# Performance work log

Measured on AMD Instinct MI355X. Metric: run time of the kernel, lower is better.

## Reference

```python
import jax, jax.numpy as jnp
import numpy as np

BANDWIDTH = 512.0


def _pairwise_lse(A, B, bandwidth):
    """logsumexp over all pairs of exp(-||a-b||^2 / bandwidth).

    Matches torch: vmap over rows b of B computing logsumexp over A,
    then logsumexp over those row results == single logsumexp over the
    full [Na, Nb] matrix of -sq_dist/bandwidth.
    """
    # squared distances via ||a||^2 + ||b||^2 - 2 a.b  (GEMM-dominated)
    a2 = jnp.sum(A * A, axis=-1)  # [Na]
    b2 = jnp.sum(B * B, axis=-1)  # [Nb]
    d2 = a2[:, None] + b2[None, :] - 2.0 * (A @ B.T)  # [Na, Nb]
    return jax.nn.logsumexp(-d2 / bandwidth)


def setup_inputs() -> dict:
    key = jax.random.key(0)
    kx, ky = jax.random.split(key)
    X = jax.random.normal(kx, (8192, 512), dtype=jnp.float32)
    Y = jax.random.normal(ky, (8192, 512), dtype=jnp.float32)
    return {"X": X, "Y": Y}


def reference(X, Y):
    n = X.shape[0]
    m = Y.shape[0]
    xx = (jnp.exp(_pairwise_lse(X, X, BANDWIDTH)) - n) / (n * (n - 1))
    xy = jnp.exp(_pairwise_lse(X, Y, BANDWIDTH)) / (n * m)
    yy = (jnp.exp(_pairwise_lse(Y, Y, BANDWIDTH)) - m) / (m * (m - 1))
    return xx - 2.0 * xy + yy
```

## Files before the change

### kernel.cpp

```cpp
#include <hip/hip_runtime.h>
#include <math.h>


#define D      512
#define BTM    128
#define BTN    256
#define BK     16
#define KSTEPS (D / BK)

#define AHI 0
#define ALO 256
#define BHI 512
#define BLO 1024

typedef _Float16 half8 __attribute__((ext_vector_type(8)));
typedef __attribute__((ext_vector_type(8)))  short  short8;
typedef __attribute__((ext_vector_type(16))) float  f32x16;

union U4H8 { uint4 u; half8 h; };
union U4S8 { uint4 u; short8 s; };

__device__ __forceinline__ unsigned short bf16_rne(float x) {
    unsigned u = __float_as_uint(x);
    return (unsigned short)((u + 0x7fffu + ((u >> 16) & 1u)) >> 16);
}
__device__ __forceinline__ float bf16_f32(unsigned short b) {
    return __uint_as_float(((unsigned)b) << 16);
}
__device__ __forceinline__ void split8(const float v[8], uint4& hi, uint4& lo) {
    unsigned h[8], l[8];
    #pragma unroll
    for (int j = 0; j < 8; j++) {
        unsigned short bh = bf16_rne(v[j]);
        float r = v[j] - bf16_f32(bh);
        unsigned short bl = bf16_rne(r);
        h[j] = bh; l[j] = bl;
    }
    hi.x = h[0] | (h[1] << 16); hi.y = h[2] | (h[3] << 16);
    hi.z = h[4] | (h[5] << 16); hi.w = h[6] | (h[7] << 16);
    lo.x = l[0] | (l[1] << 16); lo.y = l[2] | (l[3] << 16);
    lo.z = l[4] | (l[5] << 16); lo.w = l[6] | (l[7] << 16);
}

__device__ __forceinline__ void lds16(const uint4* g, uint4* l) {
    __builtin_amdgcn_global_load_lds(
        (const __attribute__((address_space(1))) void*)g,
        (__attribute__((address_space(3))) void*)(unsigned int)(uintptr_t)(void*)l,
        16, 0, 0);
}

__global__ __launch_bounds__(256)
void convert_h_kernel(const float* __restrict__ src, uint4* __restrict__ dst, int npts) {
    const int ks = blockIdx.y;
    const int p  = blockIdx.x * 256 + threadIdx.x;
    if (p >= npts) return;
    const float* s = src + (size_t)p * D + ks * BK;
    float v[16];
    *(float4*)&v[0]  = *(const float4*)(s);
    *(float4*)&v[4]  = *(const float4*)(s + 4);
    *(float4*)&v[8]  = *(const float4*)(s + 8);
    *(float4*)&v[12] = *(const float4*)(s + 12);
    U4H8 a, b;
    #pragma unroll
    for (int j = 0; j < 8; j++) { a.h[j] = (_Float16)v[j]; b.h[j] = (_Float16)v[8 + j]; }
    size_t u = (size_t)ks * npts * 2 + (size_t)(p >> 5) * 64 + (p & 31);
    dst[u] = a.u; dst[u + 32] = b.u;
}

__global__ __launch_bounds__(256)
void row_norms_kernel(const float* __restrict__ X, const float* __restrict__ Y,
                      float* __restrict__ X2, float* __restrict__ Y2, int N, int M) {
    const int wave = threadIdx.x >> 6;
    const int lane = threadIdx.x & 63;
    const int row  = blockIdx.x * 4 + wave;
    const float* src; float* dst; int r;
    if (row < N)          { src = X; dst = X2; r = row; }
    else if (row < N + M) { src = Y; dst = Y2; r = row - N; }
    else return;
    const float* p = src + (size_t)r * D;
    float s = 0.f;
    #pragma unroll
    for (int c = 0; c < D; c += 64) {
        float v = p[c + lane];
        s = fmaf(v, v, s);
    }
    #pragma unroll
    for (int off = 32; off > 0; off >>= 1) s += __shfl_down(s, off);
    if (lane == 0) dst[r] = s;
}

__device__ inline unsigned float_key(float f) {
    unsigned u = __float_as_uint(f);
    return (u & 0x80000000u) ? ~u : (u | 0x80000000u);
}
__device__ inline float key_float(unsigned k) {
    return __uint_as_float((k & 0x80000000u) ? (k ^ 0x80000000u) : ~k);
}

__global__ __launch_bounds__(256)
void diag_min_bits_kernel(const float* __restrict__ src, const float* __restrict__ n2,
                          unsigned* __restrict__ minkey, int zidx) {
    const int tid  = threadIdx.x;
    const int wave = tid >> 6, lane = tid & 63;
    const int grp  = blockIdx.x * 4 + wave;
    const int fp   = lane & 31, fh = lane >> 5;
    const int pt   = grp * 32 + fp;
    const float* s = src + (size_t)pt * D + fh * 8;

    f32x16 acc;
    #pragma unroll
    for (int i = 0; i < 16; i++) acc[i] = 0.f;

    for (int ks = 0; ks < KSTEPS; ks++) {
        float v[8];
        *(float4*)&v[0] = *(const float4*)(s + ks * BK);
        *(float4*)&v[4] = *(const float4*)(s + ks * BK + 4);
        U4S8 hi, lo;
        split8(v, hi.u, lo.u);
        short8 ah = hi.s, al = lo.s;
        acc = __builtin_amdgcn_mfma_f32_32x32x16_bf16(ah, ah, acc, 0, 0, 0);
        acc = __builtin_amdgcn_mfma_f32_32x32x16_bf16(ah, al, acc, 0, 0, 0);
        acc = __builtin_amdgcn_mfma_f32_32x32x16_bf16(al, ah, acc, 0, 0, 0);
    }

    float dmin = 1e30f;
    if (fh == ((fp >> 2) & 1)) {
        int r = (fp & 3) + 4 * (fp >> 3);
        float av = acc[r];
        float rn = n2[pt];
        float cn = rn;
        float d2 = rn + cn - 2.0f * av;
        dmin = d2;
    }
    #pragma unroll
    for (int off = 32; off > 0; off >>= 1) dmin = fminf(dmin, __shfl_down(dmin, off));
    __shared__ float wm[4];
    if (lane == 0) wm[wave] = dmin;
    __syncthreads();
    if (tid == 0)
        atomicMin(&minkey[zidx],
                  float_key(fminf(fminf(wm[0], wm[1]), fminf(wm[2], wm[3]))));
}

struct AF { half8 h[2]; };

__global__ __launch_bounds__(256, 2)
void pair_exp_sum_kernel(const uint4* __restrict__ Xh, const uint4* __restrict__ Yh,
                         const float* __restrict__ X2, const float* __restrict__ Y2,
                         double* __restrict__ accum, float* __restrict__ bmin,
                         int N, int M) {
    const int z = blockIdx.z;
    const uint4 *Ah, *Bh; const float *An, *Bn; bool sym; int na, nb;
    if (z == 0)      { Ah = Xh; Bh = Xh; An = X2; Bn = X2; sym = true;  na = N; nb = N; }
    else if (z == 1) { Ah = Xh; Bh = Yh; An = X2; Bn = Y2; sym = false; na = N; nb = M; }
    else             { Ah = Yh; Bh = Yh; An = Y2; Bn = Y2; sym = true;  na = M; nb = M; }
    const int bi = blockIdx.x, bj = blockIdx.y;
    if (sym && (2 * bj + 1) < bi) return;

    __shared__ uint4  smem[2][512];
    __shared__ float  smN[BTM + BTN];
    __shared__ double wsum[4];
    __shared__ float  wmin[4];

    const int tid  = threadIdx.x;
    const int wave = tid >> 6, lane = tid & 63;
    const int wy = wave >> 1, wx = wave & 1;
    const int row0 = bi * BTM, col0 = bj * BTN;

    if (tid < BTM) smN[tid] = An[row0 + tid];
    smN[BTM + tid] = Bn[col0 + tid];

    const int wl = wave * 64 + lane;
    const size_t strideA = (size_t)na * 2;
    const size_t strideB = (size_t)nb * 2;
    const uint4* gB0 = Bh + (size_t)(col0 >> 5) * 64 + wl;
    const uint4* gB1 = gB0 + 256;
    const half8* gA0 = (const half8*)Ah + ((size_t)(row0 >> 5) + 2 * wy) * 64 + lane;
    const half8* gA1 = gA0 + 64;

    f32x16 acc[2][4];
    #pragma unroll
    for (int g = 0; g < 2; g++)
        #pragma unroll
        for (int c = 0; c < 4; c++)
            #pragma unroll
            for (int i = 0; i < 16; i++) acc[g][c][i] = 0.f;

    auto stage = [&](int buf, int ks) {
        lds16(gB0 + (size_t)ks * strideB, &smem[buf][wl]);
        lds16(gB1 + (size_t)ks * strideB, &smem[buf][256 + wl]);
    };
    auto loadA = [&](int ks, AF& f) {
        f.h[0] = gA0[(size_t)ks * strideA];
        f.h[1] = gA1[(size_t)ks * strideA];
    };
    auto compute = [&](int buf, const AF& a) {
        const half8* p = (const half8*)&smem[buf][0];
        half8 bh[4];
        #pragma unroll
        for (int c = 0; c < 4; c++) bh[c] = p[(4 * wx + c) * 64 + lane];
        #pragma unroll
        for (int g = 0; g < 2; g++)
            #pragma unroll
            for (int c = 0; c < 4; c++)
                acc[g][c] = __builtin_amdgcn_mfma_f32_32x32x16_f16(a.h[g], bh[c], acc[g][c], 0, 0, 0);
    };

    AF A0, A1;
    stage(0, 0);
    loadA(0, A0);
    __syncthreads();

    for (int ks = 1; ks < KSTEPS - 1; ks += 2) {
        stage(1, ks);      loadA(ks, A1);
        compute(0, A0);
        __syncthreads();
        stage(0, ks + 1);  loadA(ks + 1, A0);
        compute(1, A1);
        __syncthreads();
    }
    stage(1, KSTEPS - 1);  loadA(KSTEPS - 1, A1);
    compute(0, A0);
    __syncthreads();
    compute(1, A1);

    float wgt = 1.f;
    if (sym) {
        int cblk = 2 * bj + wx;
        wgt = (cblk > bi) ? 2.f : (cblk == bi ? 1.f : 0.f);
    }

    const int fp = lane & 31, fh = lane >> 5;
    double s = 0.0;
    float dmin = 1e30f;
    if (wgt != 0.f) {
        const float* rowN = &smN[64 * wy];
        const float* colN = &smN[BTM + 128 * wx];
        const float kC = -0.0028177637517362567f;
        #pragma unroll
        for (int g = 0; g < 2; g++)
            #pragma unroll
            for (int c = 0; c < 4; c++) {
                float cn = colN[32 * c + fp];
                float rs = 0.f;
                #pragma unroll
                for (int r = 0; r < 16; r++) {
                    int r32 = (r & 3) + 8 * (r >> 2) + 4 * fh;
                    float d2 = rowN[32 * g + r32] + cn - 2.0f * acc[g][c][r];
                    dmin = fminf(dmin, d2);
                    rs += exp2f(d2 * kC);
                }
                s += (double)rs;
            }
        s *= (double)wgt;
    }

    #pragma unroll
    for (int off = 32; off > 0; off >>= 1) {
        s += __shfl_down(s, off);
        dmin = fminf(dmin, __shfl_down(dmin, off));
    }
    if (lane == 0) { wsum[wave] = s; wmin[wave] = dmin; }
    __syncthreads();
    if (tid == 0) {
        atomicAdd(&accum[z], wsum[0] + wsum[1] + wsum[2] + wsum[3]);
        if (z == 1)
            bmin[bi * gridDim.y + bj] = fminf(fminf(wmin[0], wmin[1]),
                                              fminf(wmin[2], wmin[3]));
    }
}

__global__ __launch_bounds__(256)
void xy_gmin_kernel(const float* __restrict__ bmin, float* __restrict__ gmin, int nblk) {
    float m = 1e30f;
    for (int i = threadIdx.x; i < nblk; i += 256) m = fminf(m, bmin[i]);
    #pragma unroll
    for (int off = 32; off > 0; off >>= 1) m = fminf(m, __shfl_down(m, off));
    __shared__ float wm[4];
    if ((threadIdx.x & 63) == 0) wm[threadIdx.x >> 6] = m;
    __syncthreads();
    if (threadIdx.x == 0) gmin[0] = fminf(fminf(wm[0], wm[1]), fminf(wm[2], wm[3]));
}

__global__ __launch_bounds__(256)
void refine_min_kernel(const float* __restrict__ A, const float* __restrict__ B,
                       const float* __restrict__ An, const float* __restrict__ Bn,
                       const float* __restrict__ bmin, const float* __restrict__ gmin,
                       unsigned* __restrict__ minkey, int zidx) {
    const int bi = blockIdx.x;
    const int bj = blockIdx.y;
    if (!(bmin[bi * gridDim.y + bj] < gmin[0] + 0.5f)) return;
    const int row0 = bi * BTM, col0 = bj * BTN;

    __shared__ uint4 smem[1536];
    __shared__ float smN[BTM + BTN];
    __shared__ float wmin[4];

    const int tid  = threadIdx.x;
    const int wave = tid >> 6, lane = tid & 63;
    const int wy = wave >> 1, wx = wave & 1;
    if (tid < BTM) smN[tid] = An[row0 + tid];
    smN[BTM + tid] = Bn[col0 + tid];

    const int fp = lane & 31, fh = lane >> 5;
    int au[2], bu[4];
    #pragma unroll
    for (int g = 0; g < 2; g++) au[g] = (64 * wy + 32 * g + fp) * 2 + fh;
    #pragma unroll
    for (int c = 0; c < 4; c++) bu[c] = (128 * wx + 32 * c + fp) * 2 + fh;

    f32x16 acc[2][4];
    #pragma unroll
    for (int g = 0; g < 2; g++)
        #pragma unroll
        for (int c = 0; c < 4; c++)
            #pragma unroll
            for (int i = 0; i < 16; i++) acc[g][c][i] = 0.f;

    for (int ks = 0; ks < KSTEPS; ks++) {
        __syncthreads();
        {
            const float* s = A + (size_t)(row0 + (tid >> 1)) * D + ks * BK + (tid & 1) * 8;
            float v[8];
            *(float4*)&v[0] = *(const float4*)s;
            *(float4*)&v[4] = *(const float4*)(s + 4);
            uint4 hi, lo; split8(v, hi, lo);
            smem[AHI + tid] = hi; smem[ALO + tid] = lo;
        }
        #pragma unroll
        for (int t = 0; t < 2; t++) {
            int u = tid + t * 256;
            const float* s = B + (size_t)(col0 + (u >> 1)) * D + ks * BK + (u & 1) * 8;
            float v[8];
            *(float4*)&v[0] = *(const float4*)s;
            *(float4*)&v[4] = *(const float4*)(s + 4);
            uint4 hi, lo; split8(v, hi, lo);
            smem[BHI + u] = hi; smem[BLO + u] = lo;
        }
        __syncthreads();
        {
            const short8* p = (const short8*)&smem[0];
            short8 ah[2], al[2], bh[4], bl[4];
            #pragma unroll
            for (int g = 0; g < 2; g++) { ah[g] = p[AHI + au[g]]; al[g] = p[ALO + au[g]]; }
            #pragma unroll
            for (int c = 0; c < 4; c++) { bh[c] = p[BHI + bu[c]]; bl[c] = p[BLO + bu[c]]; }
            #pragma unroll
            for (int g = 0; g < 2; g++)
                #pragma unroll
                for (int c = 0; c < 4; c++)
                    acc[g][c] = __builtin_amdgcn_mfma_f32_32x32x16_bf16(ah[g], bh[c], acc[g][c], 0, 0, 0);
            #pragma unroll
            for (int g = 0; g < 2; g++)
                #pragma unroll
                for (int c = 0; c < 4; c++)
                    acc[g][c] = __builtin_amdgcn_mfma_f32_32x32x16_bf16(ah[g], bl[c], acc[g][c], 0, 0, 0);
            #pragma unroll
            for (int g = 0; g < 2; g++)
                #pragma unroll
                for (int c = 0; c < 4; c++)
                    acc[g][c] = __builtin_amdgcn_mfma_f32_32x32x16_bf16(al[g], bh[c], acc[g][c], 0, 0, 0);
        }
    }

    float dmin = 1e30f;
    const float* rowN = &smN[64 * wy];
    const float* colN = &smN[BTM + 128 * wx];
    #pragma unroll
    for (int g = 0; g < 2; g++)
        #pragma unroll
        for (int c = 0; c < 4; c++) {
            float cn = colN[32 * c + fp];
            #pragma unroll
            for (int r = 0; r < 16; r++) {
                int r32 = (r & 3) + 8 * (r >> 2) + 4 * fh;
                float d2 = rowN[32 * g + r32] + cn - 2.0f * acc[g][c][r];
                dmin = fminf(dmin, d2);
            }
        }

    #pragma unroll
    for (int off = 32; off > 0; off >>= 1) dmin = fminf(dmin, __shfl_down(dmin, off));
    if (lane == 0) wmin[wave] = dmin;
    __syncthreads();
    if (tid == 0)
        atomicMin(&minkey[zidx],
                  float_key(fminf(fminf(wmin[0], wmin[1]), fminf(wmin[2], wmin[3]))));
}

__global__ void finalize_kernel(const double* __restrict__ accum,
                                const unsigned* __restrict__ minkey,
                                float* __restrict__ out, int N, int M) {
    if (threadIdx.x == 0 && blockIdx.x == 0) {
        float Sp[3];
        #pragma unroll
        for (int z = 0; z < 3; z++) {
            float m = key_float(minkey[z]) * (-1.0f / 512.0f);
            double Sshift = accum[z] * exp(-(double)m);
            float r = (float)log(Sshift);
            float lse = r + m;
            Sp[z] = (float)exp((double)lse);
        }
        float nf  = (float)N, mf = (float)M;
        float nn1 = (float)((double)N * (double)(N - 1));
        float mm1 = (float)((double)M * (double)(M - 1));
        float nm  = (float)((double)N * (double)M);
        float xx = (Sp[0] - nf) / nn1;
        float xy =  Sp[1]       / nm;
        float yy = (Sp[2] - mf) / mm1;
        out[0] = xx - 2.0f * xy + yy;
    }
}

extern "C" void kernel_launch(void* const* d_in, const int* in_sizes, int n_in,
                              void* d_out, int out_size, void* d_ws, size_t ws_size,
                              hipStream_t stream) {
    const float* X = (const float*)d_in[0];
    const float* Y = (const float*)d_in[1];
    const int N = in_sizes[0] / D;
    const int M = in_sizes[1] / D;
    const int gx = N / BTM, gy = M / BTN;

    double*   accum  = (double*)d_ws;
    unsigned* minkey = (unsigned*)((char*)d_ws + 32);
    float*    gmin   = (float*)((char*)d_ws + 48);
    float*    X2     = (float*)((char*)d_ws + 64);
    float*    Y2     = X2 + N;
    float*    bmin   = Y2 + M;
    size_t off = (64 + (size_t)(N + M) * 4 + (size_t)gx * gy * 4 + 255) & ~(size_t)255;
    size_t asz = (size_t)N * D * 2;
    uint4* Xh = (uint4*)((char*)d_ws + off);
    uint4* Yh = (uint4*)((char*)d_ws + off + asz);

    hipMemsetAsync(accum, 0, 32, stream);
    hipMemsetAsync(minkey, 0xFF, 16, stream);

    row_norms_kernel<<<(N + M + 3) / 4, 256, 0, stream>>>(X, Y, X2, Y2, N, M);
    convert_h_kernel<<<dim3((N + 255) / 256, KSTEPS), 256, 0, stream>>>(X, Xh, N);
    convert_h_kernel<<<dim3((M + 255) / 256, KSTEPS), 256, 0, stream>>>(Y, Yh, M);

    diag_min_bits_kernel<<<N / 128, 256, 0, stream>>>(X, X2, minkey, 0);
    diag_min_bits_kernel<<<M / 128, 256, 0, stream>>>(Y, Y2, minkey, 2);

    dim3 grid(gx, gy, 3);
    pair_exp_sum_kernel<<<grid, 256, 0, stream>>>(Xh, Yh, X2, Y2, accum, bmin, N, M);

    xy_gmin_kernel<<<1, 256, 0, stream>>>(bmin, gmin, gx * gy);
    refine_min_kernel<<<dim3(gx, gy), 256, 0, stream>>>(X, Y, X2, Y2, bmin, gmin,
                                                        minkey, 1);

    finalize_kernel<<<1, 64, 0, stream>>>(accum, minkey, (float*)d_out, N, M);
}
```

Measured before the change: 364.0 us.

## Merge setup launches and stage two K-steps per barrier in pair kernel

Replaces the two memsets with a single init kernel and merges the per-input convert and diagonal-min launches into one launch each using the grid index to pick X or Y. This cuts launch count and fixed per-launch overhead. Separately, the main pair kernel now stages two K-steps of B into doubled LDS buffers and holds four A fragments, halving the number of barriers per K loop. The trade-off is more LDS and registers per block, which may reduce occupancy under the two-blocks-per-CU bound.

```diff
diff --git a/kernel.cpp b/kernel.cpp
--- a/kernel.cpp
+++ b/kernel.cpp
@@ -49,8 +49,16 @@
         16, 0, 0);
 }
 
+__global__ void init_kernel(double* accum, unsigned* minkey) {
+    if (threadIdx.x < 3) accum[threadIdx.x] = 0.0;
+    if (threadIdx.x < 4) minkey[threadIdx.x] = 0xFFFFFFFFu;
+}
+
 __global__ __launch_bounds__(256)
-void convert_h_kernel(const float* __restrict__ src, uint4* __restrict__ dst, int npts) {
+void convert_h_kernel(const float* __restrict__ X, const float* __restrict__ Y,
+                      uint4* __restrict__ Xh, uint4* __restrict__ Yh, int npts) {
+    const float* src = blockIdx.z ? Y : X;
+    uint4*       dst = blockIdx.z ? Yh : Xh;
     const int ks = blockIdx.y;
     const int p  = blockIdx.x * 256 + threadIdx.x;
     if (p >= npts) return;
@@ -98,11 +106,17 @@
 }
 
 __global__ __launch_bounds__(256)
-void diag_min_bits_kernel(const float* __restrict__ src, const float* __restrict__ n2,
-                          unsigned* __restrict__ minkey, int zidx) {
+void diag_min_bits_kernel(const float* __restrict__ X, const float* __restrict__ Y,
+                          const float* __restrict__ X2, const float* __restrict__ Y2,
+                          unsigned* __restrict__ minkey, int ngx) {
+    int b = blockIdx.x;
+    const float *src, *n2; int zidx;
+    if (b < ngx) { src = X; n2 = X2; zidx = 0; }
+    else         { src = Y; n2 = Y2; zidx = 2; b -= ngx; }
+
     const int tid  = threadIdx.x;
     const int wave = tid >> 6, lane = tid & 63;
-    const int grp  = blockIdx.x * 4 + wave;
+    const int grp  = b * 4 + wave;
     const int fp   = lane & 31, fh = lane >> 5;
     const int pt   = grp * 32 + fp;
     const float* s = src + (size_t)pt * D + fh * 8;
@@ -135,14 +149,13 @@
     #pragma unroll
     for (int off = 32; off > 0; off >>= 1) dmin = fminf(dmin, __shfl_down(dmin, off));
     __shared__ float wm[4];
-    if (lane == 0) wm[wave] = dmin;
+    __shared__ int   wz[4];
+    if (lane == 0) { wm[wave] = dmin; wz[wave] = zidx; }
     __syncthreads();
     if (tid == 0)
-        atomicMin(&minkey[zidx],
+        atomicMin(&minkey[wz[0]],
                   float_key(fminf(fminf(wm[0], wm[1]), fminf(wm[2], wm[3]))));
 }
-
-struct AF { half8 h[2]; };
 
 __global__ __launch_bounds__(256, 2)
 void pair_exp_sum_kernel(const uint4* __restrict__ Xh, const uint4* __restrict__ Yh,
@@ -157,7 +170,7 @@
     const int bi = blockIdx.x, bj = blockIdx.y;
     if (sym && (2 * bj + 1) < bi) return;
 
-    __shared__ uint4  smem[2][512];
+    __shared__ uint4  smem[2][1024];
     __shared__ float  smN[BTM + BTN];
     __shared__ double wsum[4];
     __shared__ float  wmin[4];
@@ -186,16 +199,21 @@
             #pragma unroll
             for (int i = 0; i < 16; i++) acc[g][c][i] = 0.f;
 
-    auto stage = [&](int buf, int ks) {
-        lds16(gB0 + (size_t)ks * strideB, &smem[buf][wl]);
-        lds16(gB1 + (size_t)ks * strideB, &smem[buf][256 + wl]);
+    auto stage2 = [&](int buf, int ks) {
+        lds16(gB0 + (size_t)ks * strideB,       &smem[buf][wl]);
+        lds16(gB1 + (size_t)ks * strideB,       &smem[buf][256 + wl]);
+        lds16(gB0 + (size_t)(ks + 1) * strideB, &smem[buf][512 + wl]);
+        lds16(gB1 + (size_t)(ks + 1) * strideB, &smem[buf][768 + wl]);
     };
-    auto loadA = [&](int ks, AF& f) {
-        f.h[0] = gA0[(size_t)ks * strideA];
-        f.h[1] = gA1[(size_t)ks * strideA];
+    half8 Af[4][2];
+    auto loadA2 = [&](int ks, int s) {
+        Af[s][0]     = gA0[(size_t)ks * strideA];
+        Af[s][1]     = gA1[(size_t)ks * strideA];
+        Af[s + 1][0] = gA0[(size_t)(ks + 1) * strideA];
+        Af[s + 1][1] = gA1[(size_t)(ks + 1) * strideA];
     };
-    auto compute = [&](int buf, const AF& a) {
-        const half8* p = (const half8*)&smem[buf][0];
+    auto computeK = [&](const uint4* base, int slot) {
+        const half8* p = (const half8*)base;
         half8 bh[4];
         #pragma unroll
         for (int c = 0; c < 4; c++) bh[c] = p[(4 * wx + c) * 64 + lane];
@@ -203,26 +221,23 @@
         for (int g = 0; g < 2; g++)
             #pragma unroll
             for (int c = 0; c < 4; c++)
-                acc[g][c] = __builtin_amdgcn_mfma_f32_32x32x16_f16(a.h[g], bh[c], acc[g][c], 0, 0, 0);
+                acc[g][c] = __builtin_amdgcn_mfma_f32_32x32x16_f16(Af[slot][g], bh[c], acc[g][c], 0, 0, 0);
     };
 
-    AF A0, A1;
-    stage(0, 0);
-    loadA(0, A0);
+    stage2(0, 0);
+    loadA2(0, 0);
     __syncthreads();
 
-    for (int ks = 1; ks < KSTEPS - 1; ks += 2) {
-        stage(1, ks);      loadA(ks, A1);
-        compute(0, A0);
+    #pragma unroll
+    for (int it = 1; it < KSTEPS / 2; it++) {
+        stage2(it & 1, 2 * it);
+        loadA2(2 * it, (it & 1) * 2);
+        computeK(&smem[(it - 1) & 1][0],   ((it - 1) & 1) * 2);
+        computeK(&smem[(it - 1) & 1][512], ((it - 1) & 1) * 2 + 1);
         __syncthreads();
-        stage(0, ks + 1);  loadA(ks + 1, A0);
-        compute(1, A1);
-        __syncthreads();
-    }
-    stage(1, KSTEPS - 1);  loadA(KSTEPS - 1, A1);
-    compute(0, A0);
-    __syncthreads();
-    compute(1, A1);
+    }
+    computeK(&smem[1][0],   2);
+    computeK(&smem[1][512], 3);
 
     float wgt = 1.f;
     if (sym) {
@@ -432,15 +447,12 @@
     uint4* Xh = (uint4*)((char*)d_ws + off);
     uint4* Yh = (uint4*)((char*)d_ws + off + asz);
 
-    hipMemsetAsync(accum, 0, 32, stream);
-    hipMemsetAsync(minkey, 0xFF, 16, stream);
+    init_kernel<<<1, 64, 0, stream>>>(accum, minkey);
 
     row_norms_kernel<<<(N + M + 3) / 4, 256, 0, stream>>>(X, Y, X2, Y2, N, M);
-    convert_h_kernel<<<dim3((N + 255) / 256, KSTEPS), 256, 0, stream>>>(X, Xh, N);
-    convert_h_kernel<<<dim3((M + 255) / 256, KSTEPS), 256, 0, stream>>>(Y, Yh, M);
-
-    diag_min_bits_kernel<<<N / 128, 256, 0, stream>>>(X, X2, minkey, 0);
-    diag_min_bits_kernel<<<M / 128, 256, 0, stream>>>(Y, Y2, minkey, 2);
+    convert_h_kernel<<<dim3((N + 255) / 256, KSTEPS, 2), 256, 0, stream>>>(X, Y, Xh, Yh, N);
+
+    diag_min_bits_kernel<<<N / 128 + M / 128, 256, 0, stream>>>(X, Y, X2, Y2, minkey, N / 128);
 
     dim3 grid(gx, gy, 3);
     pair_exp_sum_kernel<<<grid, 256, 0, stream>>>(Xh, Yh, X2, Y2, accum, bmin, N, M);
```

After: 324.8 us. 1.12x faster.
